# Optimization experiments

Hardware: AMD Instinct MI355X
Metric: run time of the kernel (lower is better)

The kernel has to match this reference:

```python
import jax, jax.numpy as jnp
import numpy as np

NUM_EXPERTS = 32
TOP_K = 4
HIDDEN = 1024
FFN = 2048
BATCH, SEQ = 1, 1024


def setup_inputs() -> dict:
    key = jax.random.key(0)
    ks = jax.random.split(key, 4)
    s = 0.02
    return {
        "x": jax.random.normal(ks[0], (BATCH, SEQ, HIDDEN), jnp.float32),
        "gate_w": jax.random.normal(ks[1], (HIDDEN, NUM_EXPERTS), jnp.float32) * s,
        "gate_b": jnp.zeros((NUM_EXPERTS,), jnp.float32),
        "w1": jax.random.normal(ks[2], (NUM_EXPERTS, HIDDEN, FFN), jnp.float32) * s,
        "b1": jnp.zeros((NUM_EXPERTS, FFN), jnp.float32),
        "w2": jax.random.normal(ks[3], (NUM_EXPERTS, FFN, HIDDEN), jnp.float32) * s,
        "b2": jnp.zeros((NUM_EXPERTS, HIDDEN), jnp.float32),
        "load_ema": jnp.ones((NUM_EXPERTS,), jnp.float32) / NUM_EXPERTS,
        "top_k": TOP_K,
    }


def reference(x, gate_w, gate_b, w1, b1, w2, b2, load_ema, top_k):
    # x: [B, S, d]; eval-mode CompoundMoELayer forward.
    B, S, d = x.shape
    E = gate_w.shape[1]
    flat = x.reshape(-1, d)                              # [N, d]
    N = flat.shape[0]

    # --- router: gate logits -> top-k -> softmax over selected logits ---
    logits = flat @ gate_w + gate_b                      # [N, E]
    top_vals, top_idx = jax.lax.top_k(logits, top_k)     # [N, k]
    weights = jax.nn.softmax(top_vals, axis=-1)          # [N, k]

    # --- switch-style load-balance aux loss ---
    probs = jax.nn.softmax(logits, axis=-1)              # [N, E]
    counts = jax.nn.one_hot(top_idx, E, dtype=flat.dtype).sum(axis=1)  # [N, E]
    frac = counts.mean(axis=0) / top_k                   # [E] routed fraction
    base_aux = E * jnp.sum(frac * probs.mean(axis=0))

    # --- dense combine weights [N, E]: zero for non-selected experts ---
    comb = jnp.zeros((N, E), flat.dtype).at[jnp.arange(N)[:, None], top_idx].add(weights)

    # --- per-expert FFN (GELU, exact erf as torch default), combined ---
    def step(acc, p):
        W1, bb1, W2, bb2, ce = p                         # ce: [N] combine weight
        h = jax.nn.gelu(flat @ W1 + bb1, approximate=False)
        y = h @ W2 + bb2
        return acc + ce[:, None] * y, None

    out, _ = jax.lax.scan(step, jnp.zeros_like(flat), (w1, b1, w2, b2, comb.T))

    # --- compound entropy regularizer over expert load EMA buffer ---
    lp = load_ema / (load_ema.sum() + 1e-8)
    entropy = -jnp.sum(lp * jnp.log(lp + 1e-8))
    reg = jnp.log(jnp.asarray(E, flat.dtype)) - entropy
    aux = base_aux + 0.001 * reg
    return out.reshape(B, S, d), aux
```

## Files before the change

kernel.cpp:

```cpp
#include <hip/hip_runtime.h>
#include <hip/hip_bf16.h>
#include <cmath>

#define N_TOK 1024
#define DIM   1024
#define FFN   2048
#define NE    32
#define TOPK  4
#define TM    192
#define TN    64
#define BK    32
#define BS_STRIDE 40

typedef __attribute__((ext_vector_type(8))) short bf16x8;
typedef __attribute__((ext_vector_type(4))) float f32x4;

#define GLOBAL_AS __attribute__((address_space(1)))
#define LDS_AS    __attribute__((address_space(3)))

__device__ __forceinline__ void g2lds16(const void* g, void* l) {
    __builtin_amdgcn_global_load_lds((const GLOBAL_AS void*)g, (LDS_AS void*)l, 16, 0, 0);
}

__global__ void zero_kernel(float4* __restrict__ p) {
    p[blockIdx.x * 256 + threadIdx.x] = float4{0.f, 0.f, 0.f, 0.f};
}

__global__ __launch_bounds__(256) void router_kernel(
        const float* __restrict__ x, const float* __restrict__ gw,
        const float* __restrict__ gb, float* __restrict__ probs_mat,
        int* __restrict__ top_idx, float* __restrict__ top_w,
        __hip_bfloat16* __restrict__ xb) {
    __shared__ float part[8][32];
    int t = threadIdx.x;
    int token = blockIdx.x;
    const float* xr = x + (size_t)token * DIM;
    {
        float4 v = *(const float4*)&xr[t * 4];
        union { __hip_bfloat16 h[4]; ushort4 u; } pk;
        pk.h[0] = __float2bfloat16(v.x); pk.h[1] = __float2bfloat16(v.y);
        pk.h[2] = __float2bfloat16(v.z); pk.h[3] = __float2bfloat16(v.w);
        *(ushort4*)&xb[(size_t)token * DIM + t * 4] = pk.u;
    }
    int e = t & 31, p = t >> 5;
    float acc = 0.f;
    int i0 = p * (DIM / 8);
    for (int i = 0; i < DIM / 8; ++i)
        acc += xr[i0 + i] * gw[(size_t)(i0 + i) * NE + e];
    part[p][e] = acc;
    __syncthreads();
    if (t < 64) {
        float l = -3e38f;
        if (t < 32) {
            l = gb[t];
            for (int q = 0; q < 8; ++q) l += part[q][t];
        }
        float m = l;
        for (int off = 32; off >= 1; off >>= 1) m = fmaxf(m, __shfl_xor(m, off, 64));
        float ex = (t < 32) ? expf(l - m) : 0.f;
        float den = ex;
        for (int off = 32; off >= 1; off >>= 1) den += __shfl_xor(den, off, 64);
        if (t < 32) probs_mat[(size_t)token * 32 + t] = ex / den;
        float v = l;
        float vals[TOPK]; int idxs[TOPK];
        for (int r = 0; r < TOPK; ++r) {
            float mv = v;
            for (int off = 32; off >= 1; off >>= 1) mv = fmaxf(mv, __shfl_xor(mv, off, 64));
            unsigned long long mask = __ballot(v == mv);
            int idx = __ffsll((unsigned long long)(mask & 0xffffffffull)) - 1;
            vals[r] = mv; idxs[r] = idx;
            if (t == idx) v = -3e38f;
        }
        if (t == 0) {
            float w[TOPK]; float ss = 0.f;
            for (int r = 0; r < TOPK; ++r) { w[r] = expf(vals[r] - vals[0]); ss += w[r]; }
            for (int r = 0; r < TOPK; ++r) {
                top_idx[token * TOPK + r] = idxs[r];
                top_w[token * TOPK + r] = w[r] / ss;
            }
        }
    }
}

__global__ void aux_kernel(const float* __restrict__ probs_mat, const int* __restrict__ top_idx,
                           const float* __restrict__ load_ema, int* __restrict__ offsets,
                           int* __restrict__ cursors, float* __restrict__ out_aux) {
    __shared__ int cnt_s[32];
    __shared__ float ps[32];
    __shared__ float psum_part[8][32];
    int t = threadIdx.x;
    if (t < 32) cnt_s[t] = 0;
    __syncthreads();
    for (int i = t; i < N_TOK * TOPK; i += 256) atomicAdd(&cnt_s[top_idx[i]], 1);
    int e = t & 31, p = t >> 5;
    float s = 0.f;
    for (int tok = p; tok < N_TOK; tok += 8) s += probs_mat[(size_t)tok * 32 + e];
    psum_part[p][e] = s;
    __syncthreads();
    if (t < 32) {
        float tot = 0.f;
        for (int q = 0; q < 8; ++q) tot += psum_part[q][t];
        ps[t] = tot;
    }
    __syncthreads();
    if (t == 0) {
        int off = 0;
        for (int i = 0; i < 32; ++i) { offsets[i] = off; cursors[i] = off; off += cnt_s[i]; }
        offsets[32] = off;
        float base = 0.f;
        for (int i = 0; i < 32; ++i) {
            float frac = (float)cnt_s[i] / (float)(N_TOK * TOPK);
            base += frac * (ps[i] / (float)N_TOK);
        }
        base *= (float)NE;
        float sum_ema = 0.f;
        for (int i = 0; i < 32; ++i) sum_ema += load_ema[i];
        float H = 0.f;
        for (int i = 0; i < 32; ++i) {
            float lp = load_ema[i] / (sum_ema + 1e-8f);
            H -= lp * logf(lp + 1e-8f);
        }
        *out_aux = base + 0.001f * (logf((float)NE) - H);
    }
}

__global__ void scatter_kernel(const int* __restrict__ top_idx, const float* __restrict__ top_w,
                               int* __restrict__ cursors,
                               int* __restrict__ pair_token, float* __restrict__ pair_w) {
    int token = blockIdx.x * 256 + threadIdx.x;
    if (token >= N_TOK) return;
    for (int s = 0; s < TOPK; ++s) {
        int e = top_idx[token * TOPK + s];
        int pos = atomicAdd(&cursors[e], 1);
        pair_token[pos] = token;
        pair_w[pos] = top_w[token * TOPK + s];
    }
}

__global__ __launch_bounds__(256, 4) void gemm1_kernel(
        const __hip_bfloat16* __restrict__ xb, const float* __restrict__ w1,
        const float* __restrict__ b1, const int* __restrict__ offsets,
        const int* __restrict__ pair_token, __hip_bfloat16* __restrict__ h) {
    int e = blockIdx.z;
    int m0 = offsets[e], Me = offsets[e + 1] - m0;
    if (Me <= 0) return;
    int f0 = blockIdx.x * TN;

    __shared__ __attribute__((aligned(16))) short As[2][4 * TM * 8];
    __shared__ __attribute__((aligned(16))) __hip_bfloat16 Bs[2][TN * BS_STRIDE];
    __shared__ int toks[TM];

    int t = threadIdx.x;
    int w = t >> 6, ln = t & 63;
    int q = ln >> 4, lj = ln & 15;
    int bn = ln, bkb = w * 8;

    float bias[4];
#pragma unroll
    for (int ns = 0; ns < 4; ++ns) bias[ns] = b1[(size_t)e * FFN + f0 + ns * 16 + lj];

    const float* bbase = w1 + ((size_t)e * DIM + bkb) * FFN + f0 + bn;

    for (int mb = 0; mb < Me; mb += TM) {
        int mlim = Me - mb; if (mlim > TM) mlim = TM;
        __syncthreads();
        if (t < TM) {
            int r = t < mlim ? t : mlim - 1;
            toks[t] = pair_token[m0 + mb + r];
        }
        __syncthreads();

        float br[8];
#pragma unroll
        for (int j = 0; j < 8; ++j) br[j] = bbase[(size_t)j * FFN];
#pragma unroll
        for (int c = 0; c < 3; ++c)
            g2lds16(xb + (size_t)toks[c * 64 + ln] * DIM + w * 8,
                    &As[0][(w * TM + c * 64) * 8]);
        {
            union { __hip_bfloat16 hb[8]; int4 v; } u;
#pragma unroll
            for (int j = 0; j < 8; ++j) u.hb[j] = __float2bfloat16(br[j]);
            *(int4*)&Bs[0][bn * BS_STRIDE + bkb] = u.v;
        }
        __syncthreads();

        f32x4 acc[3][4] = {};
        int cur = 0;
        for (int k0 = 0; k0 < DIM; k0 += BK) {
            int nxt = cur ^ 1;
            bool hasNext = (k0 + BK < DIM);
            if (hasNext) {
#pragma unroll
                for (int j = 0; j < 8; ++j) br[j] = bbase[(size_t)(k0 + BK + j) * FFN];
#pragma unroll
                for (int c = 0; c < 3; ++c)
                    g2lds16(xb + (size_t)toks[c * 64 + ln] * DIM + k0 + BK + w * 8,
                            &As[nxt][(w * TM + c * 64) * 8]);
            }
            bf16x8 af[3], bfr[4];
#pragma unroll
            for (int ms = 0; ms < 3; ++ms)
                af[ms] = *(const bf16x8*)&As[cur][(q * TM + w * 48 + ms * 16 + lj) * 8];
#pragma unroll
            for (int ns = 0; ns < 4; ++ns)
                bfr[ns] = *(const bf16x8*)&Bs[cur][(ns * 16 + lj) * BS_STRIDE + q * 8];
#pragma unroll
            for (int ms = 0; ms < 3; ++ms)
#pragma unroll
                for (int ns = 0; ns < 4; ++ns)
                    acc[ms][ns] = __builtin_amdgcn_mfma_f32_16x16x32_bf16(af[ms], bfr[ns], acc[ms][ns], 0, 0, 0);
            if (hasNext) {
                union { __hip_bfloat16 hb[8]; int4 v; } u;
#pragma unroll
                for (int j = 0; j < 8; ++j) u.hb[j] = __float2bfloat16(br[j]);
                *(int4*)&Bs[nxt][bn * BS_STRIDE + bkb] = u.v;
            }
            __syncthreads();
            cur = nxt;
        }
#pragma unroll
        for (int ms = 0; ms < 3; ++ms) {
#pragma unroll
            for (int rr = 0; rr < 4; ++rr) {
                int rit = w * 48 + ms * 16 + q * 4 + rr;
                if (rit >= mlim) continue;
                size_t rowG = (size_t)(m0 + mb + rit);
#pragma unroll
                for (int ns = 0; ns < 4; ++ns) {
                    float v = acc[ms][ns][rr] + bias[ns];
                    float g = 0.5f * v * (1.f + erff(v * 0.70710678118654752f));
                    h[rowG * FFN + f0 + ns * 16 + lj] = __float2bfloat16(g);
                }
            }
        }
    }
}

__global__ __launch_bounds__(256, 4) void gemm2_kernel(
        const __hip_bfloat16* __restrict__ h, const float* __restrict__ w2,
        const float* __restrict__ b2, const int* __restrict__ offsets,
        const int* __restrict__ pair_token, const float* __restrict__ pair_w,
        float* __restrict__ out) {
    int e = blockIdx.z;
    int m0 = offsets[e], Me = offsets[e + 1] - m0;
    if (Me <= 0) return;
    int d0 = blockIdx.x * TN;
    int kbase = blockIdx.y * (FFN / 2);

    __shared__ __attribute__((aligned(16))) short As[2][4 * TM * 8];
    __shared__ __attribute__((aligned(16))) __hip_bfloat16 Bs[2][TN * BS_STRIDE];

    int t = threadIdx.x;
    int w = t >> 6, ln = t & 63;
    int q = ln >> 4, lj = ln & 15;
    int bn = ln, bkb = w * 8;

    float bias[4];
#pragma unroll
    for (int ns = 0; ns < 4; ++ns)
        bias[ns] = (blockIdx.y == 0) ? b2[(size_t)e * DIM + d0 + ns * 16 + lj] : 0.f;

    const float* bbase = w2 + ((size_t)e * FFN + kbase + bkb) * DIM + d0 + bn;

    for (int mb = 0; mb < Me; mb += TM) {
        int mlim = Me - mb; if (mlim > TM) mlim = TM;
        __syncthreads();

        float br[8];
#pragma unroll
        for (int j = 0; j < 8; ++j) br[j] = bbase[(size_t)j * DIM];
#pragma unroll
        for (int c = 0; c < 3; ++c) {
            int rit = c * 64 + ln;
            int r = rit < mlim ? rit : mlim - 1;
            g2lds16(h + (size_t)(m0 + mb + r) * FFN + kbase + w * 8,
                    &As[0][(w * TM + c * 64) * 8]);
        }
        {
            union { __hip_bfloat16 hb[8]; int4 v; } u;
#pragma unroll
            for (int j = 0; j < 8; ++j) u.hb[j] = __float2bfloat16(br[j]);
            *(int4*)&Bs[0][bn * BS_STRIDE + bkb] = u.v;
        }
        __syncthreads();

        f32x4 acc[3][4] = {};
        int cur = 0;
        for (int k0 = 0; k0 < FFN / 2; k0 += BK) {
            int nxt = cur ^ 1;
            bool hasNext = (k0 + BK < FFN / 2);
            if (hasNext) {
#pragma unroll
                for (int j = 0; j < 8; ++j) br[j] = bbase[(size_t)(k0 + BK + j) * DIM];
#pragma unroll
                for (int c = 0; c < 3; ++c) {
                    int rit = c * 64 + ln;
                    int r = rit < mlim ? rit : mlim - 1;
                    g2lds16(h + (size_t)(m0 + mb + r) * FFN + kbase + k0 + BK + w * 8,
                            &As[nxt][(w * TM + c * 64) * 8]);
                }
            }
            bf16x8 af[3], bfr[4];
#pragma unroll
            for (int ms = 0; ms < 3; ++ms)
                af[ms] = *(const bf16x8*)&As[cur][(q * TM + w * 48 + ms * 16 + lj) * 8];
#pragma unroll
            for (int ns = 0; ns < 4; ++ns)
                bfr[ns] = *(const bf16x8*)&Bs[cur][(ns * 16 + lj) * BS_STRIDE + q * 8];
#pragma unroll
            for (int ms = 0; ms < 3; ++ms)
#pragma unroll
                for (int ns = 0; ns < 4; ++ns)
                    acc[ms][ns] = __builtin_amdgcn_mfma_f32_16x16x32_bf16(af[ms], bfr[ns], acc[ms][ns], 0, 0, 0);
            if (hasNext) {
                union { __hip_bfloat16 hb[8]; int4 v; } u;
#pragma unroll
                for (int j = 0; j < 8; ++j) u.hb[j] = __float2bfloat16(br[j]);
                *(int4*)&Bs[nxt][bn * BS_STRIDE + bkb] = u.v;
            }
            __syncthreads();
            cur = nxt;
        }
#pragma unroll
        for (int ms = 0; ms < 3; ++ms) {
#pragma unroll
            for (int rr = 0; rr < 4; ++rr) {
                int rit = w * 48 + ms * 16 + q * 4 + rr;
                if (rit >= mlim) continue;
                int pr = m0 + mb + rit;
                int tok = pair_token[pr];
                float wgt = pair_w[pr];
#pragma unroll
                for (int ns = 0; ns < 4; ++ns)
                    atomicAdd(&out[(size_t)tok * DIM + d0 + ns * 16 + lj],
                              wgt * (acc[ms][ns][rr] + bias[ns]));
            }
        }
    }
}

extern "C" void kernel_launch(void* const* d_in, const int* in_sizes, int n_in,
                              void* d_out, int out_size, void* d_ws, size_t ws_size,
                              hipStream_t stream) {
    const float* x        = (const float*)d_in[0];
    const float* gate_w   = (const float*)d_in[1];
    const float* gate_b   = (const float*)d_in[2];
    const float* w1       = (const float*)d_in[3];
    const float* b1       = (const float*)d_in[4];
    const float* w2       = (const float*)d_in[5];
    const float* b2       = (const float*)d_in[6];
    const float* load_ema = (const float*)d_in[7];
    float* out = (float*)d_out;

    char* base = (char*)d_ws;
    size_t off = 0;
    auto alloc = [&](size_t bytes) {
        void* p = base + off;
        off = (off + bytes + 255) & ~(size_t)255;
        return p;
    };
    float* probs_mat = (float*)alloc(N_TOK * 32 * sizeof(float));
    int*   top_idx   = (int*)  alloc(N_TOK * TOPK * sizeof(int));
    float* top_w     = (float*)alloc(N_TOK * TOPK * sizeof(float));
    int*   offsets   = (int*)  alloc(33 * sizeof(int));
    int*   cursors   = (int*)  alloc(32 * sizeof(int));
    int*   pair_token= (int*)  alloc(N_TOK * TOPK * sizeof(int));
    float* pair_w    = (float*)alloc(N_TOK * TOPK * sizeof(float));
    __hip_bfloat16* xb = (__hip_bfloat16*)alloc((size_t)N_TOK * DIM * sizeof(__hip_bfloat16));
    __hip_bfloat16* h  = (__hip_bfloat16*)alloc((size_t)N_TOK * TOPK * FFN * sizeof(__hip_bfloat16));

    zero_kernel<<<N_TOK * DIM / (256 * 4), 256, 0, stream>>>((float4*)out);
    router_kernel<<<N_TOK, 256, 0, stream>>>(x, gate_w, gate_b, probs_mat, top_idx, top_w, xb);
    aux_kernel<<<1, 256, 0, stream>>>(probs_mat, top_idx, load_ema, offsets, cursors,
                                      out + (size_t)N_TOK * DIM);
    scatter_kernel<<<(N_TOK + 255) / 256, 256, 0, stream>>>(top_idx, top_w, cursors,
                                                            pair_token, pair_w);
    {
        dim3 grid(FFN / TN, 1, NE);
        gemm1_kernel<<<grid, 256, 0, stream>>>(xb, w1, b1, offsets, pair_token, h);
    }
    {
        dim3 grid(DIM / TN, 2, NE);
        gemm2_kernel<<<grid, 256, 0, stream>>>(h, w2, b2, offsets, pair_token, pair_w, out);
    }
}
```

Before: 676.4 us.

## Deepen GEMM prefetch pipeline to two stages with explicit vmcnt waits

Both expert GEMM kernels now keep two K-tiles of global loads in flight: fp32 weight registers are double-buffered and the LDS A-tile loads are issued two iterations ahead. Fine-grained s_waitcnt vmcnt counts and sched_barrier fences replace the plain __syncthreads, so loads overlap the MFMA work instead of being fully drained each step. Token and row indices are hoisted into registers. In exchange the code depends on the compiler issuing memory operations in exactly the expected order, uses more registers, and redundantly reloads the last tile near the end of the loop.

```diff
diff --git a/kernel.cpp b/kernel.cpp
--- a/kernel.cpp
+++ b/kernel.cpp
@@ -21,6 +21,12 @@
 __device__ __forceinline__ void g2lds16(const void* g, void* l) {
     __builtin_amdgcn_global_load_lds((const GLOBAL_AS void*)g, (LDS_AS void*)l, 16, 0, 0);
 }
+
+#define PIPE_BAR() do { asm volatile("s_waitcnt lgkmcnt(0)" ::: "memory"); \
+                        __builtin_amdgcn_s_barrier(); \
+                        __builtin_amdgcn_sched_barrier(0); } while (0)
+#define WAIT_VM(n) asm volatile("s_waitcnt vmcnt(" #n ")" ::: "memory")
+#define SCHED_FENCE() __builtin_amdgcn_sched_barrier(0)
 
 __global__ void zero_kernel(float4* __restrict__ p) {
     p[blockIdx.x * 256 + threadIdx.x] = float4{0.f, 0.f, 0.f, 0.f};
@@ -137,6 +143,12 @@
     }
 }
 
+#define LOADB(kk, br, STRIDE) { _Pragma("unroll") \
+    for (int j = 0; j < 8; ++j) (br)[j] = bbase[(size_t)((kk) + j) * (STRIDE)]; }
+#define WRITEB(br, buf) { union { __hip_bfloat16 hb[8]; int4 v; } u; _Pragma("unroll") \
+    for (int j = 0; j < 8; ++j) u.hb[j] = __float2bfloat16((br)[j]); \
+    *(int4*)&Bs[buf][bn * BS_STRIDE + bkb] = u.v; }
+
 __global__ __launch_bounds__(256, 4) void gemm1_kernel(
         const __hip_bfloat16* __restrict__ xb, const float* __restrict__ w1,
         const float* __restrict__ b1, const int* __restrict__ offsets,
@@ -161,6 +173,11 @@
 
     const float* bbase = w1 + ((size_t)e * DIM + bkb) * FFN + f0 + bn;
 
+#define STAGEA1(kk, buf) { \
+    g2lds16(xb + (size_t)tok0 * DIM + (kk) + w * 8, &As[buf][(w * TM +   0) * 8]); \
+    g2lds16(xb + (size_t)tok1 * DIM + (kk) + w * 8, &As[buf][(w * TM +  64) * 8]); \
+    g2lds16(xb + (size_t)tok2 * DIM + (kk) + w * 8, &As[buf][(w * TM + 128) * 8]); }
+
     for (int mb = 0; mb < Me; mb += TM) {
         int mlim = Me - mb; if (mlim > TM) mlim = TM;
         __syncthreads();
@@ -169,55 +186,44 @@
             toks[t] = pair_token[m0 + mb + r];
         }
         __syncthreads();
-
-        float br[8];
-#pragma unroll
-        for (int j = 0; j < 8; ++j) br[j] = bbase[(size_t)j * FFN];
-#pragma unroll
-        for (int c = 0; c < 3; ++c)
-            g2lds16(xb + (size_t)toks[c * 64 + ln] * DIM + w * 8,
-                    &As[0][(w * TM + c * 64) * 8]);
-        {
-            union { __hip_bfloat16 hb[8]; int4 v; } u;
-#pragma unroll
-            for (int j = 0; j < 8; ++j) u.hb[j] = __float2bfloat16(br[j]);
-            *(int4*)&Bs[0][bn * BS_STRIDE + bkb] = u.v;
-        }
-        __syncthreads();
+        int tok0 = toks[ln], tok1 = toks[64 + ln], tok2 = toks[128 + ln];
+
+        float br0[8], br1[8];
+        LOADB(0, br0, FFN);  SCHED_FENCE();
+        STAGEA1(0, 0);       SCHED_FENCE();
+        LOADB(BK, br1, FFN); SCHED_FENCE();
+        STAGEA1(BK, 1);      SCHED_FENCE();
+        WAIT_VM(14);
+        WRITEB(br0, 0);
+        WAIT_VM(11);
+        PIPE_BAR();
 
         f32x4 acc[3][4] = {};
-        int cur = 0;
-        for (int k0 = 0; k0 < DIM; k0 += BK) {
-            int nxt = cur ^ 1;
-            bool hasNext = (k0 + BK < DIM);
-            if (hasNext) {
-#pragma unroll
-                for (int j = 0; j < 8; ++j) br[j] = bbase[(size_t)(k0 + BK + j) * FFN];
-#pragma unroll
-                for (int c = 0; c < 3; ++c)
-                    g2lds16(xb + (size_t)toks[c * 64 + ln] * DIM + k0 + BK + w * 8,
-                            &As[nxt][(w * TM + c * 64) * 8]);
-            }
+#pragma unroll 2
+        for (int i = 0; i < DIM / BK; ++i) {
+            int p = i & 1;
             bf16x8 af[3], bfr[4];
 #pragma unroll
             for (int ms = 0; ms < 3; ++ms)
-                af[ms] = *(const bf16x8*)&As[cur][(q * TM + w * 48 + ms * 16 + lj) * 8];
+                af[ms] = *(const bf16x8*)&As[p][(q * TM + w * 48 + ms * 16 + lj) * 8];
 #pragma unroll
             for (int ns = 0; ns < 4; ++ns)
-                bfr[ns] = *(const bf16x8*)&Bs[cur][(ns * 16 + lj) * BS_STRIDE + q * 8];
+                bfr[ns] = *(const bf16x8*)&Bs[p][(ns * 16 + lj) * BS_STRIDE + q * 8];
+            PIPE_BAR();
+            int kpre = (i + 2 < DIM / BK) ? (i + 2) * BK : DIM - BK;
+            if (p == 0) { LOADB(kpre, br0, FFN); } else { LOADB(kpre, br1, FFN); }
+            SCHED_FENCE();
+            STAGEA1(kpre, p);
+            SCHED_FENCE();
 #pragma unroll
             for (int ms = 0; ms < 3; ++ms)
 #pragma unroll
                 for (int ns = 0; ns < 4; ++ns)
                     acc[ms][ns] = __builtin_amdgcn_mfma_f32_16x16x32_bf16(af[ms], bfr[ns], acc[ms][ns], 0, 0, 0);
-            if (hasNext) {
-                union { __hip_bfloat16 hb[8]; int4 v; } u;
-#pragma unroll
-                for (int j = 0; j < 8; ++j) u.hb[j] = __float2bfloat16(br[j]);
-                *(int4*)&Bs[nxt][bn * BS_STRIDE + bkb] = u.v;
-            }
-            __syncthreads();
-            cur = nxt;
+            WAIT_VM(14);
+            if (p == 0) { WRITEB(br1, 1); } else { WRITEB(br0, 0); }
+            WAIT_VM(11);
+            PIPE_BAR();
         }
 #pragma unroll
         for (int ms = 0; ms < 3; ++ms) {
@@ -235,6 +241,7 @@
             }
         }
     }
+#undef STAGEA1
 }
 
 __global__ __launch_bounds__(256, 4) void gemm2_kernel(
@@ -263,64 +270,54 @@
 
     const float* bbase = w2 + ((size_t)e * FFN + kbase + bkb) * DIM + d0 + bn;
 
+#define STAGEA2(kk, buf) { \
+    g2lds16(h + (size_t)r0 * FFN + kbase + (kk) + w * 8, &As[buf][(w * TM +   0) * 8]); \
+    g2lds16(h + (size_t)r1 * FFN + kbase + (kk) + w * 8, &As[buf][(w * TM +  64) * 8]); \
+    g2lds16(h + (size_t)r2 * FFN + kbase + (kk) + w * 8, &As[buf][(w * TM + 128) * 8]); }
+
     for (int mb = 0; mb < Me; mb += TM) {
         int mlim = Me - mb; if (mlim > TM) mlim = TM;
         __syncthreads();
-
-        float br[8];
-#pragma unroll
-        for (int j = 0; j < 8; ++j) br[j] = bbase[(size_t)j * DIM];
-#pragma unroll
-        for (int c = 0; c < 3; ++c) {
-            int rit = c * 64 + ln;
-            int r = rit < mlim ? rit : mlim - 1;
-            g2lds16(h + (size_t)(m0 + mb + r) * FFN + kbase + w * 8,
-                    &As[0][(w * TM + c * 64) * 8]);
-        }
-        {
-            union { __hip_bfloat16 hb[8]; int4 v; } u;
-#pragma unroll
-            for (int j = 0; j < 8; ++j) u.hb[j] = __float2bfloat16(br[j]);
-            *(int4*)&Bs[0][bn * BS_STRIDE + bkb] = u.v;
-        }
-        __syncthreads();
+        int r0 = m0 + mb + (ln       < mlim ? ln       : mlim - 1);
+        int r1 = m0 + mb + (64 + ln  < mlim ? 64 + ln  : mlim - 1);
+        int r2 = m0 + mb + (128 + ln < mlim ? 128 + ln : mlim - 1);
+
+        float br0[8], br1[8];
+        LOADB(0, br0, DIM);  SCHED_FENCE();
+        STAGEA2(0, 0);       SCHED_FENCE();
+        LOADB(BK, br1, DIM); SCHED_FENCE();
+        STAGEA2(BK, 1);      SCHED_FENCE();
+        WAIT_VM(14);
+        WRITEB(br0, 0);
+        WAIT_VM(11);
+        PIPE_BAR();
 
         f32x4 acc[3][4] = {};
-        int cur = 0;
-        for (int k0 = 0; k0 < FFN / 2; k0 += BK) {
-            int nxt = cur ^ 1;
-            bool hasNext = (k0 + BK < FFN / 2);
-            if (hasNext) {
-#pragma unroll
-                for (int j = 0; j < 8; ++j) br[j] = bbase[(size_t)(k0 + BK + j) * DIM];
-#pragma unroll
-                for (int c = 0; c < 3; ++c) {
-                    int rit = c * 64 + ln;
-                    int r = rit < mlim ? rit : mlim - 1;
-                    g2lds16(h + (size_t)(m0 + mb + r) * FFN + kbase + k0 + BK + w * 8,
-                            &As[nxt][(w * TM + c * 64) * 8]);
-                }
-            }
+#pragma unroll 2
+        for (int i = 0; i < (FFN / 2) / BK; ++i) {
+            int p = i & 1;
             bf16x8 af[3], bfr[4];
 #pragma unroll
             for (int ms = 0; ms < 3; ++ms)
-                af[ms] = *(const bf16x8*)&As[cur][(q * TM + w * 48 + ms * 16 + lj) * 8];
+                af[ms] = *(const bf16x8*)&As[p][(q * TM + w * 48 + ms * 16 + lj) * 8];
 #pragma unroll
             for (int ns = 0; ns < 4; ++ns)
-                bfr[ns] = *(const bf16x8*)&Bs[cur][(ns * 16 + lj) * BS_STRIDE + q * 8];
+                bfr[ns] = *(const bf16x8*)&Bs[p][(ns * 16 + lj) * BS_STRIDE + q * 8];
+            PIPE_BAR();
+            int kpre = (i + 2 < (FFN / 2) / BK) ? (i + 2) * BK : (FFN / 2) - BK;
+            if (p == 0) { LOADB(kpre, br0, DIM); } else { LOADB(kpre, br1, DIM); }
+            SCHED_FENCE();
+            STAGEA2(kpre, p);
+            SCHED_FENCE();
 #pragma unroll
             for (int ms = 0; ms < 3; ++ms)
 #pragma unroll
                 for (int ns = 0; ns < 4; ++ns)
                     acc[ms][ns] = __builtin_amdgcn_mfma_f32_16x16x32_bf16(af[ms], bfr[ns], acc[ms][ns], 0, 0, 0);
-            if (hasNext) {
-                union { __hip_bfloat16 hb[8]; int4 v; } u;
-#pragma unroll
-                for (int j = 0; j < 8; ++j) u.hb[j] = __float2bfloat16(br[j]);
-                *(int4*)&Bs[nxt][bn * BS_STRIDE + bkb] = u.v;
-            }
-            __syncthreads();
-            cur = nxt;
+            WAIT_VM(14);
+            if (p == 0) { WRITEB(br1, 1); } else { WRITEB(br0, 0); }
+            WAIT_VM(11);
+            PIPE_BAR();
         }
 #pragma unroll
         for (int ms = 0; ms < 3; ++ms) {
@@ -338,6 +335,7 @@
             }
         }
     }
+#undef STAGEA2
 }
 
 extern "C" void kernel_launch(void* const* d_in, const int* in_sizes, int n_in,
```

Result: slower. 707.5 us (+4.6%).
